# Kernel tuning notes

Measured on AMD Instinct MI355X. Metric: run time of the kernel, lower is better.

Reference implementation:

```python
import jax, jax.numpy as jnp
import numpy as np

N, CIN, COUT, K, S, H, W = 16, 512, 512, 3, 512, 64, 64
EPS = 1e-8


def setup_inputs() -> dict:
    key = jax.random.key(0)
    k1, k2, k3, k4 = jax.random.split(key, 4)
    return {
        "x": jax.random.normal(k1, (N, CIN, H, W), jnp.float32),
        "style": jax.random.normal(k2, (N, S), jnp.float32),
        # conv weight ~ N(0,1) as in the torch module (lr_mul=1)
        "weight": jax.random.normal(k3, (COUT, CIN, K, K), jnp.float32),
        # style modulation linear: weight ~ N(0,1), bias init 1.0
        "style_w": jax.random.normal(k4, (CIN, S), jnp.float32),
        "style_b": jnp.ones((CIN,), jnp.float32),
    }


def reference(x, style, weight, style_w, style_b):
    # equalized-lr scales (gain=1.0, lr_mul=1.0, mode=fan_in)
    lin_scale = 1.0 / jnp.sqrt(jnp.float32(S))          # fan_in of linear = style_channels
    w_scale = 1.0 / jnp.sqrt(jnp.float32(CIN * K * K))  # fan_in of weight[0] = Cin*k*k

    # style modulation: s[n, cin] (style_bias = 0.0)
    s = style @ (style_w.T * lin_scale) + style_b        # [N, Cin]

    w = weight * w_scale                                  # [Cout, Cin, K, K]

    # demodulation: rsqrt(sum_{i,kh,kw} (w[o,i]*s[n,i])^2 + eps) per (n, o)
    demod = jax.lax.rsqrt(jnp.einsum('oikl,ni->no', w * w, s * s) + EPS)  # [N, Cout]

    # fused form: conv(x * s, W) * demod  ==  grouped conv with per-sample modulated weights
    xs = x * s[:, :, None, None]
    out = jax.lax.conv_general_dilated(
        xs, w, window_strides=(1, 1), padding='SAME',
        dimension_numbers=('NCHW', 'OIHW', 'NCHW'))
    return out * demod[:, :, None, None]
```

## Files before the change

kernel.cpp:

```cpp
#include <hip/hip_runtime.h>
#include <hip/hip_bf16.h>

#define CIN   512
#define COUT  512
#define HW    4096
#define PADW  66
#define NB    16
#define KTOT  4608
#define BUFSZ 65536
#define BOFF  32768

static constexpr float LIN_SCALE = 0.044194173824159216f;
static constexpr float W_SCALE   = 0.014731391274719738f;

typedef __attribute__((ext_vector_type(8))) short bf16x8;
typedef __attribute__((ext_vector_type(4))) float f32x4;

__device__ __forceinline__ unsigned short f2us(float f) {
    __hip_bfloat16 h = __float2bfloat16(f); unsigned short u; __builtin_memcpy(&u, &h, 2); return u;
}

typedef const __attribute__((address_space(1))) unsigned int guint;
typedef __attribute__((address_space(3))) unsigned int luint;
__device__ __forceinline__ void gload_lds16(const void* g, void* l) {
    __builtin_amdgcn_global_load_lds((guint*)g, (luint*)l, 16, 0, 0);
}

__global__ void k_prep(const float* __restrict__ weight,
                       const float* __restrict__ style,
                       const float* __restrict__ style_w,
                       const float* __restrict__ style_b,
                       float* __restrict__ wsq,
                       __hip_bfloat16* __restrict__ wt,
                       float* __restrict__ s) {
    const int bid = blockIdx.x;
    if (bid < 1024) {
        int oi = bid * 256 + threadIdx.x;
        int o = oi >> 9, i = oi & 511;
        float sq = 0.f;
#pragma unroll
        for (int tp = 0; tp < 9; ++tp) {
            float v = weight[(size_t)oi * 9 + tp] * W_SCALE;
            sq += v * v;
            wt[(size_t)o * KTOT + tp * 512 + i] = __float2bfloat16(v);
        }
        wsq[oi] = sq;
    } else {
        int wid  = (bid - 1024) * 4 + (threadIdx.x >> 6);
        int lane = threadIdx.x & 63;
        int n = wid >> 9, i = wid & 511;
        float sum = 0.f;
        for (int j = lane; j < 512; j += 64)
            sum += style[n * 512 + j] * style_w[i * 512 + j];
        for (int m = 32; m; m >>= 1) sum += __shfl_xor(sum, m, 64);
        if (lane == 0) s[n * 512 + i] = sum * LIN_SCALE + style_b[i];
    }
}

__global__ void k_xs(const float* __restrict__ x, const float* __restrict__ s,
                     __hip_bfloat16* __restrict__ xs) {
    const int n = blockIdx.y;
    const int t = threadIdx.x;
    if (blockIdx.x == 32) {
        uint4 z = make_uint4(0u, 0u, 0u, 0u);
        for (int idx = t; idx < 16640; idx += 512) {
            int bp = idx >> 6, sl = idx & 63;
            int hp, wp;
            if (bp < 66)       { hp = 0;  wp = bp; }
            else if (bp < 132) { hp = 65; wp = bp - 66; }
            else { int k2 = bp - 132; hp = 1 + (k2 >> 1); wp = (k2 & 1) ? 65 : 0; }
            *(uint4*)(xs + (((size_t)n * PADW * PADW) + hp * PADW + wp) * 512 + sl * 8) = z;
        }
        return;
    }
    const int half = t >> 8;
    const int tt   = t & 255;
    const int h    = blockIdx.x * 2 + half;
    const int PITCH = 65;
    __shared__ float lds[2][64 * 65];
    __shared__ float sv[512];
    float* ld = lds[half];
    sv[t] = s[n * 512 + t];
    for (int ic = 0; ic < 8; ++ic) {
        const int i0 = ic * 64;
        __syncthreads();
#pragma unroll
        for (int j = 0; j < 4; ++j) {
            int idx = j * 256 + tt;
            int il = idx >> 4;
            int wq = (idx & 15) * 4;
            float4 v = *(const float4*)(x + (((size_t)n * 512 + i0 + il) * HW) + h * 64 + wq);
            float* dst = &ld[il * PITCH + wq];
            dst[0] = v.x; dst[1] = v.y; dst[2] = v.z; dst[3] = v.w;
        }
        __syncthreads();
#pragma unroll
        for (int j = 0; j < 2; ++j) {
            int idx = j * 256 + tt;
            int wp = idx >> 3;
            int ib = (idx & 7) * 8;
            unsigned short tmp[8];
#pragma unroll
            for (int r = 0; r < 8; ++r) {
                float xv = ld[(ib + r) * PITCH + wp];
                tmp[r] = f2us(xv * sv[i0 + ib + r]);
            }
            uint4 o;
            o.x = (unsigned)tmp[0] | ((unsigned)tmp[1] << 16);
            o.y = (unsigned)tmp[2] | ((unsigned)tmp[3] << 16);
            o.z = (unsigned)tmp[4] | ((unsigned)tmp[5] << 16);
            o.w = (unsigned)tmp[6] | ((unsigned)tmp[7] << 16);
            *(uint4*)(xs + ((size_t)((n * PADW + h + 1) * PADW + (wp + 1))) * 512 + i0 + ib) = o;
        }
    }
}

#define BAR      __builtin_amdgcn_s_barrier()
#define WAITLGKM asm volatile("s_waitcnt lgkmcnt(0)" ::: "memory")
#define LOAD_B(CH) { _Pragma("unroll") for (int t_ = 0; t_ < 4; ++t_) \
    bfr[t_] = *(const bf16x8*)(cb + BOFF + bRow + t_ * 2048 + (CH)); }
#define LOAD_A(MG, CH) { _Pragma("unroll") for (int t_ = 0; t_ < 4; ++t_) \
    af[t_] = *(const bf16x8*)(cb + aRow + ((MG) * 4 + t_) * 2048 + (CH)); }
#define DO_MFMA(MG) { __builtin_amdgcn_s_setprio(1); \
    _Pragma("unroll") for (int m_ = 0; m_ < 4; ++m_) \
    _Pragma("unroll") for (int n_ = 0; n_ < 4; ++n_) \
        acc[(MG) * 4 + m_][n_] = __builtin_amdgcn_mfma_f32_16x16x32_bf16( \
            af[m_], bfr[n_], acc[(MG) * 4 + m_][n_], 0, 0, 0); \
    __builtin_amdgcn_s_setprio(0); }

__global__ __launch_bounds__(512, 2) void k_conv(
        const __hip_bfloat16* __restrict__ wt,
        const __hip_bfloat16* __restrict__ xs,
        const float* __restrict__ wsq,
        const float* __restrict__ s_buf,
        float* __restrict__ out) {
    __shared__ __attribute__((aligned(16))) char smem[2 * BUFSZ];
    const int tid  = threadIdx.x;
    const int wv   = tid >> 6, lane = tid & 63;
    const int wm   = wv >> 2,  wn   = wv & 3;

    const int bid = blockIdx.x;
    const int xcd = bid & 7, idx = bid >> 3;
    const int pT  = idx & 15;
    const int o0  = ((idx >> 4) & 1) * 256;
    const int smp = xcd * 2 + (idx >> 5);

    const __hip_bfloat16* xsn = xs + (size_t)smp * (PADW * PADW * 512);

    const int rw = lane >> 3, cl = lane & 7;
    const int lc = cl ^ rw;
    const size_t aOff = (size_t)(wv * 8 + rw) * KTOT + lc * 8;
    const size_t bOff = (size_t)(wv * 8 + rw) * 512  + lc * 8;
    const __hip_bfloat16* aStage = wt  + (size_t)o0 * KTOT + aOff;
    const __hip_bfloat16* bStage = xsn + bOff;

    const int col = lane & 15, qd = lane >> 4;
    const int ch0 = ((qd)     ^ (col & 7)) << 4;
    const int ch1 = ((qd + 4) ^ (col & 7)) << 4;
    const int aRow = (wm * 128 + col) * 128;
    const int bRow = (wn * 64  + col) * 128;

    f32x4 acc[8][4] = {};

    {
        char* nbB = smem + BOFF + wv * 1024;
        char* nbA = smem + wv * 1024;
        const __hip_bfloat16* bS = bStage + (size_t)(pT * 4) * 33792;
        gload_lds16(bS,              nbB);
        gload_lds16(bS + 33792,      nbB + 8192);
        gload_lds16(bS + 2 * 33792,  nbB + 2 * 8192);
        gload_lds16(bS + 3 * 33792,  nbB + 3 * 8192);
        gload_lds16(aStage,              nbA);
        gload_lds16(aStage + 2 * 294912, nbA + 2 * 8192);
        gload_lds16(aStage + 294912,     nbA + 8192);
        gload_lds16(aStage + 3 * 294912, nbA + 3 * 8192);
        asm volatile("s_waitcnt vmcnt(2)" ::: "memory");
        BAR;
    }

    for (int kt = 0; kt < 71; ++kt) {
        const char* cb = smem + (kt & 1) * BUFSZ;
        char* nb = (char*)smem + ((kt + 1) & 1) * BUFSZ;
        const int kt1  = kt + 1;
        const int tap1 = kt1 >> 3, c1 = kt1 & 7;
        const int kh1  = (tap1 * 11) >> 5;
        const int kw1  = tap1 - kh1 * 3;
        const __hip_bfloat16* aS = aStage + (size_t)kt1 * 64;
        const __hip_bfloat16* bS = bStage +
            (size_t)((pT * 4 + kh1) * PADW + kw1) * 512 + c1 * 64;
        char* nbB = nb + BOFF + wv * 1024;
        char* nbA = nb + wv * 1024;

        bf16x8 af[4], bfr[4];

        LOAD_B(ch0); LOAD_A(0, ch0);
        gload_lds16(bS,             nbB);
        gload_lds16(bS + 33792,     nbB + 8192);
        gload_lds16(bS + 2 * 33792, nbB + 2 * 8192);
        BAR; WAITLGKM;
        DO_MFMA(0);
        asm volatile("s_waitcnt vmcnt(3)" ::: "memory");
        BAR;

        LOAD_A(1, ch0);
        gload_lds16(bS + 3 * 33792, nbB + 3 * 8192);
        gload_lds16(aS,             nbA);
        gload_lds16(aS + 2 * 294912, nbA + 2 * 8192);
        BAR; WAITLGKM;
        DO_MFMA(1);
        BAR;

        LOAD_B(ch1); LOAD_A(0, ch1);
        gload_lds16(aS + 294912,     nbA + 8192);
        gload_lds16(aS + 3 * 294912, nbA + 3 * 8192);
        BAR; WAITLGKM;
        DO_MFMA(0);
        BAR;

        LOAD_A(1, ch1);
        BAR; WAITLGKM;
        DO_MFMA(1);
        asm volatile("s_waitcnt vmcnt(2)" ::: "memory");
        BAR;
    }

    {
        const char* cb = smem + BUFSZ;
        asm volatile("s_waitcnt vmcnt(0)" ::: "memory");
        BAR;
        bf16x8 af[4], bfr[4];
        LOAD_B(ch0); LOAD_A(0, ch0); DO_MFMA(0);
        LOAD_A(1, ch0);              DO_MFMA(1);
        LOAD_B(ch1); LOAD_A(0, ch1); DO_MFMA(0);
        LOAD_A(1, ch1);              DO_MFMA(1);
    }

    __syncthreads();
    float* s2  = (float*)smem;
    float* dml = (float*)(smem + 2048);
    {
        float sv = s_buf[smp * 512 + tid];
        s2[tid] = sv * sv;
    }
    __syncthreads();
#pragma unroll 4
    for (int ow = 0; ow < 32; ++ow) {
        const int o = wv * 32 + ow;
        const float* wrow = wsq + (size_t)(o0 + o) * 512;
        float sum = 0.f;
#pragma unroll
        for (int ii = 0; ii < 8; ++ii)
            sum += wrow[ii * 64 + lane] * s2[ii * 64 + lane];
        for (int m = 32; m; m >>= 1) sum += __shfl_xor(sum, m, 64);
        if (lane == 0) dml[o] = rsqrtf(sum + 1e-8f);
    }
    __syncthreads();

    const int hwBase = pT * 256 + wn * 64 + col;
#pragma unroll
    for (int m = 0; m < 8; ++m) {
#pragma unroll
        for (int rg = 0; rg < 4; ++rg) {
            const int o = o0 + wm * 128 + m * 16 + qd * 4 + rg;
            const float dm = dml[wm * 128 + m * 16 + qd * 4 + rg];
            float* orow = out + ((size_t)(smp * COUT + o)) * HW + hwBase;
#pragma unroll
            for (int nn = 0; nn < 4; ++nn)
                orow[nn * 16] = acc[m][nn][rg] * dm;
        }
    }
}

extern "C" void kernel_launch(void* const* d_in, const int* in_sizes, int n_in,
                              void* d_out, int out_size, void* d_ws, size_t ws_size,
                              hipStream_t stream) {
    const float* x       = (const float*)d_in[0];
    const float* style   = (const float*)d_in[1];
    const float* weight  = (const float*)d_in[2];
    const float* style_w = (const float*)d_in[3];
    const float* style_b = (const float*)d_in[4];
    float* out = (float*)d_out;

    char* ws = (char*)d_ws;
    float*          s_buf  = (float*)(ws + 0);
    float*          wsq    = (float*)(ws + 32768);
    __hip_bfloat16* wt     = (__hip_bfloat16*)(ws + 1114112);
    __hip_bfloat16* xs     = (__hip_bfloat16*)(ws + 5832704);

    k_prep <<<dim3(3072),    dim3(256), 0, stream>>>(weight, style, style_w, style_b,
                                                     wsq, wt, s_buf);
    k_xs   <<<dim3(33, 16),  dim3(512), 0, stream>>>(x, s_buf, xs);
    k_conv <<<dim3(512),     dim3(512), 0, stream>>>(wt, xs, wsq, s_buf, out);
}
```

Baseline: 521.0 us.

## Move demodulation computation from conv epilogue into activation-prep kernel

The per-(sample, out-channel) demodulation factor is now computed once per sample in extra blocks of the k_xs kernel and written to a workspace buffer, rather than recomputed by every conv block in its epilogue. This removes two block-wide syncs and a wsq dot-product loop from the tail of every conv block. The xs prep kernel is also reshaped to one output row per 256-thread block, which doubles the block count and halves LDS per block. The added cost is a global load of demod in the epilogue and one serial block per sample doing 512 reductions, which could become a tail in k_xs.

```diff
diff --git a/kernel.cpp b/kernel.cpp
--- a/kernel.cpp
+++ b/kernel.cpp
@@ -58,12 +58,14 @@
 }
 
 __global__ void k_xs(const float* __restrict__ x, const float* __restrict__ s,
-                     __hip_bfloat16* __restrict__ xs) {
+                     const float* __restrict__ wsq,
+                     __hip_bfloat16* __restrict__ xs,
+                     float* __restrict__ demod) {
     const int n = blockIdx.y;
     const int t = threadIdx.x;
-    if (blockIdx.x == 32) {
+    if (blockIdx.x == 64) {
         uint4 z = make_uint4(0u, 0u, 0u, 0u);
-        for (int idx = t; idx < 16640; idx += 512) {
+        for (int idx = t; idx < 16640; idx += 256) {
             int bp = idx >> 6, sl = idx & 63;
             int hp, wp;
             if (bp < 66)       { hp = 0;  wp = bp; }
@@ -73,36 +75,53 @@
         }
         return;
     }
-    const int half = t >> 8;
-    const int tt   = t & 255;
-    const int h    = blockIdx.x * 2 + half;
+    if (blockIdx.x == 65) {
+        const int wave = t >> 6, lane = t & 63;
+        float sq[8];
+#pragma unroll
+        for (int k = 0; k < 8; ++k) {
+            float sv = s[n * 512 + k * 64 + lane];
+            sq[k] = sv * sv;
+        }
+        for (int o = wave; o < 512; o += 4) {
+            const float* wrow = wsq + (size_t)o * 512;
+            float sum = 0.f;
+#pragma unroll
+            for (int k = 0; k < 8; ++k)
+                sum += wrow[k * 64 + lane] * sq[k];
+            for (int m = 32; m; m >>= 1) sum += __shfl_xor(sum, m, 64);
+            if (lane == 0) demod[n * 512 + o] = rsqrtf(sum + 1e-8f);
+        }
+        return;
+    }
+    const int h = blockIdx.x;
     const int PITCH = 65;
-    __shared__ float lds[2][64 * 65];
+    __shared__ float lds[64 * 65];
     __shared__ float sv[512];
-    float* ld = lds[half];
     sv[t] = s[n * 512 + t];
+    sv[t + 256] = s[n * 512 + 256 + t];
     for (int ic = 0; ic < 8; ++ic) {
         const int i0 = ic * 64;
         __syncthreads();
 #pragma unroll
         for (int j = 0; j < 4; ++j) {
-            int idx = j * 256 + tt;
+            int idx = j * 256 + t;
             int il = idx >> 4;
             int wq = (idx & 15) * 4;
             float4 v = *(const float4*)(x + (((size_t)n * 512 + i0 + il) * HW) + h * 64 + wq);
-            float* dst = &ld[il * PITCH + wq];
+            float* dst = &lds[il * PITCH + wq];
             dst[0] = v.x; dst[1] = v.y; dst[2] = v.z; dst[3] = v.w;
         }
         __syncthreads();
 #pragma unroll
         for (int j = 0; j < 2; ++j) {
-            int idx = j * 256 + tt;
+            int idx = j * 256 + t;
             int wp = idx >> 3;
             int ib = (idx & 7) * 8;
             unsigned short tmp[8];
 #pragma unroll
             for (int r = 0; r < 8; ++r) {
-                float xv = ld[(ib + r) * PITCH + wp];
+                float xv = lds[(ib + r) * PITCH + wp];
                 tmp[r] = f2us(xv * sv[i0 + ib + r]);
             }
             uint4 o;
@@ -131,8 +150,7 @@
 __global__ __launch_bounds__(512, 2) void k_conv(
         const __hip_bfloat16* __restrict__ wt,
         const __hip_bfloat16* __restrict__ xs,
-        const float* __restrict__ wsq,
-        const float* __restrict__ s_buf,
+        const float* __restrict__ demod,
         float* __restrict__ out) {
     __shared__ __attribute__((aligned(16))) char smem[2 * BUFSZ];
     const int tid  = threadIdx.x;
@@ -235,34 +253,13 @@
         LOAD_A(1, ch1);              DO_MFMA(1);
     }
 
-    __syncthreads();
-    float* s2  = (float*)smem;
-    float* dml = (float*)(smem + 2048);
-    {
-        float sv = s_buf[smp * 512 + tid];
-        s2[tid] = sv * sv;
-    }
-    __syncthreads();
-#pragma unroll 4
-    for (int ow = 0; ow < 32; ++ow) {
-        const int o = wv * 32 + ow;
-        const float* wrow = wsq + (size_t)(o0 + o) * 512;
-        float sum = 0.f;
-#pragma unroll
-        for (int ii = 0; ii < 8; ++ii)
-            sum += wrow[ii * 64 + lane] * s2[ii * 64 + lane];
-        for (int m = 32; m; m >>= 1) sum += __shfl_xor(sum, m, 64);
-        if (lane == 0) dml[o] = rsqrtf(sum + 1e-8f);
-    }
-    __syncthreads();
-
     const int hwBase = pT * 256 + wn * 64 + col;
 #pragma unroll
     for (int m = 0; m < 8; ++m) {
 #pragma unroll
         for (int rg = 0; rg < 4; ++rg) {
             const int o = o0 + wm * 128 + m * 16 + qd * 4 + rg;
-            const float dm = dml[wm * 128 + m * 16 + qd * 4 + rg];
+            const float dm = demod[smp * 512 + o];
             float* orow = out + ((size_t)(smp * COUT + o)) * HW + hwBase;
 #pragma unroll
             for (int nn = 0; nn < 4; ++nn)
@@ -284,11 +281,12 @@
     char* ws = (char*)d_ws;
     float*          s_buf  = (float*)(ws + 0);
     float*          wsq    = (float*)(ws + 32768);
+    float*          demod  = (float*)(ws + 1081344);
     __hip_bfloat16* wt     = (__hip_bfloat16*)(ws + 1114112);
     __hip_bfloat16* xs     = (__hip_bfloat16*)(ws + 5832704);
 
     k_prep <<<dim3(3072),    dim3(256), 0, stream>>>(weight, style, style_w, style_b,
                                                      wsq, wt, s_buf);
-    k_xs   <<<dim3(33, 16),  dim3(512), 0, stream>>>(x, s_buf, xs);
-    k_conv <<<dim3(512),     dim3(512), 0, stream>>>(wt, xs, wsq, s_buf, out);
-}
+    k_xs   <<<dim3(66, 16),  dim3(256), 0, stream>>>(x, s_buf, wsq, xs, demod);
+    k_conv <<<dim3(512),     dim3(512), 0, stream>>>(wt, xs, demod, out);
+}
```

Measured after the change: 540.8 us. +3.8%, slower.
